# Performance work log

Hardware: AMD Instinct MI355X
Metric: run time of the kernel (lower is better)

The kernel has to match this reference:

```python
import jax, jax.numpy as jnp
import numpy as np

NUM_HEADS = 8
EPS = 1e-5

def layer_norm(x, g, b):
    m = jnp.mean(x, axis=-1, keepdims=True)
    v = jnp.mean(jnp.square(x - m), axis=-1, keepdims=True)
    return (x - m) * jax.lax.rsqrt(v + EPS) * g + b

def setup_inputs() -> dict:
    key = jax.random.key(0)
    ks = jax.random.split(key, 16)
    B, C_enc, C_dec = 2, 512, 256
    H = W = D = 16
    d_ff = 4 * C_dec
    s = 0.02
    inp = {
        'encoder_feat': jax.random.normal(ks[0], (B, C_enc, H, W, D), jnp.float32),
        'decoder_feat': jax.random.normal(ks[1], (B, C_dec, H, W, D), jnp.float32),
        # projections stored as (in, out)
        'Wq': jax.random.normal(ks[2], (C_dec, C_dec), jnp.float32) * s,
        'bq': jnp.zeros((C_dec,), jnp.float32),
        'Wk': jax.random.normal(ks[3], (C_enc, C_dec), jnp.float32) * s,
        'bk': jnp.zeros((C_dec,), jnp.float32),
        'Wv': jax.random.normal(ks[4], (C_enc, C_dec), jnp.float32) * s,
        'bv': jnp.zeros((C_dec,), jnp.float32),
        'Wo': jax.random.normal(ks[5], (C_dec, C_dec), jnp.float32) * s,
        'bo': jnp.zeros((C_dec,), jnp.float32),
        'g_enc': jnp.ones((C_enc,), jnp.float32),
        'b_enc': jnp.zeros((C_enc,), jnp.float32),
        'g_dec': jnp.ones((C_dec,), jnp.float32),
        'b_dec': jnp.zeros((C_dec,), jnp.float32),
        'g_out': jnp.ones((C_dec,), jnp.float32),
        'b_out': jnp.zeros((C_dec,), jnp.float32),
        'W1': jax.random.normal(ks[6], (C_dec, d_ff), jnp.float32) * s,
        'b1': jnp.zeros((d_ff,), jnp.float32),
        'W2': jax.random.normal(ks[7], (d_ff, C_dec), jnp.float32) * s,
        'b2': jnp.zeros((C_dec,), jnp.float32),
    }
    return inp

def reference(encoder_feat, decoder_feat, Wq, bq, Wk, bk, Wv, bv, Wo, bo,
              g_enc, b_enc, g_dec, b_dec, g_out, b_out, W1, b1, W2, b2):
    B, C_dec, H, W, D = decoder_feat.shape
    h = NUM_HEADS
    hd = C_dec // h
    scale = hd ** -0.5
    # flatten spatial dims -> sequences [B, S, C]
    enc_seq = encoder_feat.reshape(B, encoder_feat.shape[1], -1).transpose(0, 2, 1)
    dec_seq = decoder_feat.reshape(B, C_dec, -1).transpose(0, 2, 1)
    enc_n = layer_norm(enc_seq, g_enc, b_enc)
    dec_n = layer_norm(dec_seq, g_dec, b_dec)
    Sq = dec_n.shape[1]
    Sk = enc_n.shape[1]
    Q = (dec_n @ Wq + bq).reshape(B, Sq, h, hd).transpose(0, 2, 1, 3)
    K = (enc_n @ Wk + bk).reshape(B, Sk, h, hd).transpose(0, 2, 1, 3)
    V = (enc_n @ Wv + bv).reshape(B, Sk, h, hd).transpose(0, 2, 1, 3)
    attn = jnp.einsum('bhqd,bhkd->bhqk', Q, K) * scale
    attn = jax.nn.softmax(attn, axis=-1)
    out = jnp.einsum('bhqk,bhkd->bhqd', attn, V)
    out = out.transpose(0, 2, 1, 3).reshape(B, Sq, C_dec)
    out = out @ Wo + bo
    out = dec_seq + out
    ffn = jax.nn.gelu(layer_norm(out, g_out, b_out) @ W1 + b1, approximate=False) @ W2 + b2
    out = out + ffn
    return out.transpose(0, 2, 1).reshape(B, C_dec, H, W, D)
```

## Files before the change

kernel.cpp:

```cpp
#include <hip/hip_runtime.h>
#include <hip/hip_bf16.h>
#include <math.h>
#include <stdint.h>

typedef __hip_bfloat16 bf16;
typedef __attribute__((ext_vector_type(8))) short short8;
typedef __attribute__((ext_vector_type(4))) short short4v;
typedef __attribute__((ext_vector_type(4))) float f32x4;
typedef __attribute__((ext_vector_type(4))) unsigned int uint32x4;
typedef __attribute__((ext_vector_type(2))) unsigned int uint32x2;

#define B_   2
#define S_   4096
#define CE   512
#define CD   256
#define DFF  1024
#define NH   8
#define HD   32

static __device__ __forceinline__ float b2f(bf16 x) { return __bfloat162float(x); }
static __device__ __forceinline__ bf16  f2b(float x) { return __float2bfloat16(x); }
static __device__ __forceinline__ short f2bs(float x) {
  bf16 h = f2b(x); return __builtin_bit_cast(short, h);
}
static __device__ __forceinline__ float s2f(short x) {
  return b2f(__builtin_bit_cast(bf16, x));
}
static __device__ __forceinline__ bool is_f32(const unsigned* graw) {
  return graw[0] == 0x3F800000u;
}

static __device__ __forceinline__ float exp2_(float x) {
#if __has_builtin(__builtin_amdgcn_exp2f)
  return __builtin_amdgcn_exp2f(x);
#else
  float r; asm("v_exp_f32 %0, %1" : "=v"(r) : "v"(x)); return r;
#endif
}
static __device__ __forceinline__ unsigned cvt_pk_bf16(float lo, float hi) {
  unsigned r;
  asm("v_cvt_pk_bf16_f32 %0, %1, %2" : "=v"(r) : "v"(lo), "v"(hi));
  return r;
}
static __device__ __forceinline__ void perm32(unsigned& a, unsigned& b) {
#if __has_builtin(__builtin_amdgcn_permlane32_swap)
  uint32x2 r = __builtin_amdgcn_permlane32_swap(a, b, false, false);
  a = r[0]; b = r[1];
#else
  asm("v_permlane32_swap_b32 %0, %1" : "+v"(a), "+v"(b));
#endif
}
static __device__ __forceinline__ void perm16(unsigned& a, unsigned& b) {
#if __has_builtin(__builtin_amdgcn_permlane16_swap)
  uint32x2 r = __builtin_amdgcn_permlane16_swap(a, b, false, false);
  a = r[0]; b = r[1];
#else
  asm("v_permlane16_swap_b32 %0, %1" : "+v"(a), "+v"(b));
#endif
}

#define GLD16(gptr, lptr) \
  __builtin_amdgcn_global_load_lds( \
      (const __attribute__((address_space(1))) unsigned int*)(gptr), \
      (__attribute__((address_space(3))) unsigned int*)(lptr), 16, 0, 0)

#define WAITVM(N) asm volatile("s_waitcnt vmcnt(" #N ")" ::: "memory")
#define BAR() __builtin_amdgcn_s_barrier()

struct PrepTab {
  const void* tsrc[6];
  bf16* tdst[6];
  int tK[6], tsStr[6], tdStr[6];
  float tscl[6];
  int tbase[7];
  const void* csrc[14];
  bf16* cdst[14];
  float cscl[14];
  int coff[15];
};

__global__ __launch_bounds__(256) void prep_kernel(
    PrepTab p, const unsigned* __restrict__ graw) {
  __shared__ bf16 tile[32][33];
  bool f32i = is_f32(graw);
  int blk = blockIdx.x;
  if (blk < p.tbase[6]) {
    int j = 0;
    #pragma unroll 1
    while (blk >= p.tbase[j + 1]) ++j;
    int local = blk - p.tbase[j];
    int ktiles = p.tK[j] >> 5;
    int nt = local / ktiles, kt = local - nt * ktiles;
    int k0 = kt * 32, n0 = nt * 32;
    const void* src = p.tsrc[j];
    bf16* dst = p.tdst[j];
    int sStr = p.tsStr[j], dStr = p.tdStr[j];
    float scl = p.tscl[j];
    int t = threadIdx.x;
    int tc = t & 31, tr = t >> 5;
    #pragma unroll
    for (int i = 0; i < 32; i += 8) {
      size_t idx = (size_t)(k0 + tr + i) * sStr + n0 + tc;
      float v = f32i ? ((const float*)src)[idx] : b2f(((const bf16*)src)[idx]);
      tile[tr + i][tc] = f2b(v * scl);
    }
    __syncthreads();
    #pragma unroll
    for (int i = 0; i < 32; i += 8)
      dst[(size_t)(n0 + tr + i) * dStr + k0 + tc] = tile[tc][tr + i];
  } else {
    int idx = (blk - p.tbase[6]) * 256 + threadIdx.x;
    int e4 = idx * 4;
    if (e4 >= p.coff[14]) return;
    int j = 0;
    #pragma unroll 1
    while (e4 >= p.coff[j + 1]) ++j;
    int local = e4 - p.coff[j];
    float v0, v1, v2, v3;
    if (f32i) {
      float4 f = *(const float4*)((const float*)p.csrc[j] + local);
      v0 = f.x; v1 = f.y; v2 = f.z; v3 = f.w;
    } else {
      short4v h = *(const short4v*)((const short*)p.csrc[j] + local);
      v0 = s2f(h[0]); v1 = s2f(h[1]); v2 = s2f(h[2]); v3 = s2f(h[3]);
    }
    float scl = p.cscl[j];
    short4v o;
    o[0] = f2bs(v0 * scl); o[1] = f2bs(v1 * scl);
    o[2] = f2bs(v2 * scl); o[3] = f2bs(v3 * scl);
    *(short4v*)((short*)p.cdst[j] + local) = o;
  }
}

struct LNCfg {
  const bf16 *x, *g, *bt;
  bf16 *xn, *xt;
  int C;
};

template<int CC, bool XT>
static __device__ __forceinline__ void ln_tile_body(
    const LNCfg& T, int b, int s0, short* sT, short* sG, short* sBt) {
  constexpr int P = CC + 8;
  constexpr int NJ = CC / 64;
  int t = threadIdx.x;
  if (t < CC / 8)      *(short8*)&sG[t * 8] = ((const short8*)T.g)[t];
  else if (t < CC / 4) *(short8*)&sBt[(t - CC/8) * 8] = ((const short8*)T.bt)[t - CC/8];

  int cg = t >> 2;
  int sq = (t & 3) * 8;
  const short* xg = (const short*)T.x + (size_t)b * CC * S_ + s0 + sq;
  short8 ld[NJ];
  #pragma unroll
  for (int ci = 0; ci < NJ; ++ci)
    ld[ci] = *(const short8*)(xg + (size_t)(ci * 64 + cg) * S_);
  #pragma unroll
  for (int ci = 0; ci < NJ; ++ci) {
    int c = ci * 64 + cg;
    #pragma unroll
    for (int j = 0; j < 8; ++j) {
      int s = sq + j;
      sT[s * P + (c ^ ((s & 24) << 1))] = ld[ci][j];
    }
  }
  __syncthreads();

  int w = t >> 6, l = t & 63;
  int grp = l >> 3, k = l & 7;
  int s = w * 8 + grp;
  int Z = (s & 24) << 1;
  short8 vals[NJ];
  float sum = 0.f, sq2 = 0.f;
  #pragma unroll
  for (int j = 0; j < NJ; ++j) {
    vals[j] = *(const short8*)&sT[s * P + j * 64 + ((k * 8) ^ Z)];
    #pragma unroll
    for (int i = 0; i < 8; ++i) {
      float v = s2f(vals[j][i]);
      sum += v; sq2 += v * v;
    }
  }
  #pragma unroll
  for (int off = 1; off < 8; off <<= 1) {
    sum += __shfl_xor(sum, off);
    sq2 += __shfl_xor(sq2, off);
  }
  float mean = sum * (1.f / CC);
  float rstd = rsqrtf(sq2 * (1.f / CC) - mean * mean + 1e-5f);
  size_t ro = ((size_t)b * S_ + s0 + s) * CC;
  #pragma unroll
  for (int j = 0; j < NJ; ++j) {
    int c0 = j * 64 + k * 8;
    short8 gv = *(const short8*)&sG[c0];
    short8 bv = *(const short8*)&sBt[c0];
    short8 o;
    #pragma unroll
    for (int i = 0; i < 8; ++i) {
      float v = s2f(vals[j][i]);
      o[i] = f2bs((v - mean) * rstd * s2f(gv[i]) + s2f(bv[i]));
    }
    *(short8*)((short*)T.xn + ro + c0) = o;
    if (XT) *(short8*)((short*)T.xt + ro + c0) = vals[j];
  }
}

__global__ __launch_bounds__(256) void ln_tile_kernel(LNCfg e, LNCfg d) {
  __shared__ __align__(16) short sT[32 * 520];
  __shared__ __align__(16) short sG[512], sBt[512];
  int gb = blockIdx.x;
  int local = gb & 255;
  int b = local >> 7, s0 = (local & 127) * 32;
  if (gb < 256) ln_tile_body<512, false>(e, b, s0, sT, sG, sBt);
  else          ln_tile_body<256, true>(d, b, s0, sT, sG, sBt);
}

__global__ __launch_bounds__(256) void ln_rows_kernel(
    const float* __restrict__ x, const bf16* __restrict__ g,
    const bf16* __restrict__ bt, bf16* __restrict__ xn, int C) {
  int wave = threadIdx.x >> 6, lane = threadIdx.x & 63;
  int row = blockIdx.x * 4 + wave;
  float4 v = *(const float4*)(x + (size_t)row * 256 + lane * 4);
  float sum = v.x + v.y + v.z + v.w;
  float sq = v.x * v.x + v.y * v.y + v.z * v.z + v.w * v.w;
  #pragma unroll
  for (int off = 1; off < 64; off <<= 1) {
    sum += __shfl_xor(sum, off);
    sq  += __shfl_xor(sq, off);
  }
  float mean = sum * (1.f / 256.f);
  float rstd = rsqrtf(sq * (1.f / 256.f) - mean * mean + 1e-5f);
  short4v gg = *(const short4v*)((const short*)g + lane * 4);
  short4v bb = *(const short4v*)((const short*)bt + lane * 4);
  short4v o;
  o[0] = f2bs((v.x - mean) * rstd * s2f(gg[0]) + s2f(bb[0]));
  o[1] = f2bs((v.y - mean) * rstd * s2f(gg[1]) + s2f(bb[1]));
  o[2] = f2bs((v.z - mean) * rstd * s2f(gg[2]) + s2f(bb[2]));
  o[3] = f2bs((v.w - mean) * rstd * s2f(gg[3]) + s2f(bb[3]));
  *(short4v*)((short*)xn + (size_t)row * 256 + lane * 4) = o;
}

__global__ __launch_bounds__(256) void gemm_mfma_kernel(
    const bf16* __restrict__ A, const bf16* __restrict__ Wt,
    const bf16* __restrict__ bias, int M, int N, int K,
    const bf16* __restrict__ resid_bf, const float* __restrict__ resid_f,
    bf16* __restrict__ out_bf, float* __restrict__ out_f,
    void* __restrict__ out_t, const unsigned* __restrict__ graw,
    int act, int resid_mode, int out_mode) {
  __shared__ __align__(16) short sA[3][128 * 32];
  __shared__ __align__(16) short sB[3][64 * 32];
  int m0 = blockIdx.y * 128, n0 = blockIdx.x * 64;
  int t = threadIdx.x;
  int w = t >> 6;
  int wm = w >> 1, wn = w & 1;
  int n16 = t & 15, quad = (t & 63) >> 4;
  int srow = t >> 2, skg = (t & 3) * 8;

  f32x4 acc[4][2] = {};
  const short* Ag = (const short*)A;
  const short* Wg = (const short*)Wt;
  const short* a0p = Ag + (size_t)(m0 + srow) * K + skg;
  const short* a1p = Ag + (size_t)(m0 + 64 + srow) * K + skg;
  const short* wp  = Wg + (size_t)(n0 + srow) * K + skg;

  auto stage = [&](int buf, int kk) {
    GLD16(a0p + kk, (char*)sA[buf] + t * 16);
    GLD16(a1p + kk, (char*)sA[buf] + t * 16 + 4096);
    GLD16(wp + kk,  (char*)sB[buf] + t * 16);
  };
  int nt = K >> 5;
  stage(0, 0);
  stage(1, 32);
  WAITVM(3);
  BAR();

  for (int ti = 0; ti < nt; ++ti) {
    int cur = ti % 3;
    bool pf = (ti + 2) < nt;
    if (pf) stage((ti + 2) % 3, (ti + 2) * 32);
    short8 af[4], bfr[2];
    #pragma unroll
    for (int ms = 0; ms < 4; ++ms)
      af[ms] = *(const short8*)&sA[cur][(wm * 64 + ms * 16 + n16) * 32 + quad * 8];
    #pragma unroll
    for (int ns = 0; ns < 2; ++ns)
      bfr[ns] = *(const short8*)&sB[cur][(wn * 32 + ns * 16 + n16) * 32 + quad * 8];
    #pragma unroll
    for (int ms = 0; ms < 4; ++ms)
      #pragma unroll
      for (int ns = 0; ns < 2; ++ns)
        acc[ms][ns] = __builtin_amdgcn_mfma_f32_16x16x32_bf16(
            af[ms], bfr[ns], acc[ms][ns], 0, 0, 0);
    if (pf) WAITVM(3); else WAITVM(0);
    BAR();
  }

  #pragma unroll
  for (int ms = 0; ms < 4; ++ms) {
    #pragma unroll
    for (int ns = 0; ns < 2; ++ns) {
      int col = n0 + wn * 32 + ns * 16 + n16;
      float bv = b2f(bias[col]);
      #pragma unroll
      for (int r = 0; r < 4; ++r) {
        int row = m0 + wm * 64 + ms * 16 + quad * 4 + r;
        float c = acc[ms][ns][r] + bv;
        if (act == 1) c = 0.5f * c * (1.f + erff(c * 0.70710678118654752f));
        size_t off = (size_t)row * N + col;
        if (resid_mode == 1)      c += b2f(resid_bf[off]);
        else if (resid_mode == 2) c += resid_f[off];
        if (out_f) out_f[off] = c;
        else       out_bf[off] = f2b(c);
      }
    }
  }
}

__global__ __launch_bounds__(256) void gemm64_mfma_kernel(
    const bf16* __restrict__ A, const bf16* __restrict__ Wt,
    const bf16* __restrict__ bias, int M, int N, int K,
    const bf16* __restrict__ resid_bf, const float* __restrict__ resid_f,
    bf16* __restrict__ out_bf, float* __restrict__ out_f,
    void* __restrict__ out_t, const unsigned* __restrict__ graw,
    int act, int resid_mode, int out_mode) {
  __shared__ __align__(16) short sA[3][64 * 32];
  __shared__ __align__(16) short sB[3][64 * 32];
  int m0 = blockIdx.y * 64, n0 = blockIdx.x * 64;
  int t = threadIdx.x;
  int w = t >> 6;
  int wm = w >> 1, wn = w & 1;
  int n16 = t & 15, quad = (t & 63) >> 4;
  int srow = t >> 2, skg = (t & 3) * 8;

  f32x4 acc[2][2] = {};
  const short* Ag = (const short*)A;
  const short* Wg = (const short*)Wt;
  const short* ap = Ag + (size_t)(m0 + srow) * K + skg;
  const short* wp = Wg + (size_t)(n0 + srow) * K + skg;

  auto stage = [&](int buf, int kk) {
    GLD16(ap + kk, (char*)sA[buf] + t * 16);
    GLD16(wp + kk, (char*)sB[buf] + t * 16);
  };
  int nt = K >> 5;
  stage(0, 0);
  stage(1, 32);
  WAITVM(2);
  BAR();

  for (int ti = 0; ti < nt; ++ti) {
    int cur = ti % 3;
    bool pf = (ti + 2) < nt;
    if (pf) stage((ti + 2) % 3, (ti + 2) * 32);
    short8 af[2], bfr[2];
    #pragma unroll
    for (int ms = 0; ms < 2; ++ms)
      af[ms] = *(const short8*)&sA[cur][(wm * 32 + ms * 16 + n16) * 32 + quad * 8];
    #pragma unroll
    for (int ns = 0; ns < 2; ++ns)
      bfr[ns] = *(const short8*)&sB[cur][(wn * 32 + ns * 16 + n16) * 32 + quad * 8];
    #pragma unroll
    for (int ms = 0; ms < 2; ++ms)
      #pragma unroll
      for (int ns = 0; ns < 2; ++ns)
        acc[ms][ns] = __builtin_amdgcn_mfma_f32_16x16x32_bf16(
            af[ms], bfr[ns], acc[ms][ns], 0, 0, 0);
    if (pf) WAITVM(2); else WAITVM(0);
    BAR();
  }

  if (out_mode == 3) {
    bool isf32 = is_f32(graw);
    #pragma unroll
    for (int ms = 0; ms < 2; ++ms) {
      int row0 = m0 + wm * 32 + ms * 16 + quad * 4;
      int bb = row0 >> 12, s = row0 & (S_ - 1);
      #pragma unroll
      for (int ns = 0; ns < 2; ++ns) {
        int col = n0 + wn * 32 + ns * 16 + n16;
        float bv = b2f(bias[col]);
        float cv[4];
        #pragma unroll
        for (int r = 0; r < 4; ++r)
          cv[r] = acc[ms][ns][r] + bv + resid_f[(size_t)(row0 + r) * N + col];
        size_t oidx = ((size_t)bb * CD + col) * S_ + s;
        if (isf32) {
          float4 v4 = {cv[0], cv[1], cv[2], cv[3]};
          *(float4*)((float*)out_t + oidx) = v4;
        } else {
          short4v v;
          #pragma unroll
          for (int r = 0; r < 4; ++r) v[r] = f2bs(cv[r]);
          *(short4v*)((bf16*)out_t + oidx) = v;
        }
      }
    }
    return;
  }

  #pragma unroll
  for (int ms = 0; ms < 2; ++ms) {
    #pragma unroll
    for (int ns = 0; ns < 2; ++ns) {
      int col = n0 + wn * 32 + ns * 16 + n16;
      float bv = b2f(bias[col]);
      #pragma unroll
      for (int r = 0; r < 4; ++r) {
        int row = m0 + wm * 32 + ms * 16 + quad * 4 + r;
        float c = acc[ms][ns][r] + bv;
        if (act == 1) c = 0.5f * c * (1.f + erff(c * 0.70710678118654752f));
        size_t off = (size_t)row * N + col;
        if (resid_mode == 1)      c += b2f(resid_bf[off]);
        else if (resid_mode == 2) c += resid_f[off];
        if (out_f) out_f[off] = c;
        else       out_bf[off] = f2b(c);
      }
    }
  }
}

__global__ __launch_bounds__(256) void qkv_kernel(
    const bf16* __restrict__ dec_n, const bf16* __restrict__ enc_n,
    const bf16* __restrict__ Wqt, const bf16* __restrict__ Wkvt,
    const bf16* __restrict__ bq, const bf16* __restrict__ bkv,
    bf16* __restrict__ Qm, bf16* __restrict__ Km, bf16* __restrict__ VT) {
  __shared__ __align__(16) short sA[3][64 * 32];
  __shared__ __align__(16) short sB[3][64 * 32];
  bool isQ = blockIdx.x < 4;
  const short* Ag = (const short*)(isQ ? dec_n : enc_n);
  const short* Wg = (const short*)(isQ ? Wqt : Wkvt);
  const bf16* bias = isQ ? bq : bkv;
  int K = isQ ? CD : CE;
  int n0 = isQ ? blockIdx.x * 64 : (blockIdx.x - 4) * 64;
  int m0 = blockIdx.y * 64;
  int t = threadIdx.x;
  int w = t >> 6;
  int wm = w >> 1, wn = w & 1;
  int n16 = t & 15, quad = (t & 63) >> 4;
  int srow = t >> 2, skg = (t & 3) * 8;

  f32x4 acc[2][2] = {};
  const short* ap = Ag + (size_t)(m0 + srow) * K + skg;
  const short* wp = Wg + (size_t)(n0 + srow) * K + skg;
  auto stage = [&](int buf, int kk) {
    GLD16(ap + kk, (char*)sA[buf] + t * 16);
    GLD16(wp + kk, (char*)sB[buf] + t * 16);
  };
  int nt = K >> 5;
  stage(0, 0);
  stage(1, 32);
  WAITVM(2);
  BAR();

  for (int ti = 0; ti < nt; ++ti) {
    int cur = ti % 3;
    bool pf = (ti + 2) < nt;
    if (pf) stage((ti + 2) % 3, (ti + 2) * 32);
    short8 af[2], bfr[2];
    #pragma unroll
    for (int ms = 0; ms < 2; ++ms)
      af[ms] = *(const short8*)&sA[cur][(wm * 32 + ms * 16 + n16) * 32 + quad * 8];
    #pragma unroll
    for (int ns = 0; ns < 2; ++ns)
      bfr[ns] = *(const short8*)&sB[cur][(wn * 32 + ns * 16 + n16) * 32 + quad * 8];
    #pragma unroll
    for (int ms = 0; ms < 2; ++ms)
      #pragma unroll
      for (int ns = 0; ns < 2; ++ns)
        acc[ms][ns] = __builtin_amdgcn_mfma_f32_16x16x32_bf16(
            af[ms], bfr[ns], acc[ms][ns], 0, 0, 0);
    if (pf) WAITVM(2); else WAITVM(0);
    BAR();
  }

  if (!isQ && n0 >= 256) {
    #pragma unroll
    for (int ms = 0; ms < 2; ++ms) {
      int row0 = m0 + wm * 32 + ms * 16 + quad * 4;
      int bb = row0 >> 12, s = row0 & (S_ - 1);
      #pragma unroll
      for (int ns = 0; ns < 2; ++ns) {
        int col = n0 + wn * 32 + ns * 16 + n16;
        float bv = b2f(bias[col]);
        short4v v;
        #pragma unroll
        for (int r = 0; r < 4; ++r) v[r] = f2bs(acc[ms][ns][r] + bv);
        *(short4v*)(VT + ((size_t)bb * CD + col - 256) * S_ + s) = v;
      }
    }
    return;
  }
  bf16* outp = isQ ? Qm : Km;
  #pragma unroll
  for (int ms = 0; ms < 2; ++ms) {
    #pragma unroll
    for (int ns = 0; ns < 2; ++ns) {
      int col = n0 + wn * 32 + ns * 16 + n16;
      float bv = b2f(bias[col]);
      #pragma unroll
      for (int r = 0; r < 4; ++r) {
        int row = m0 + wm * 32 + ms * 16 + quad * 4 + r;
        outp[(size_t)row * CD + col] = f2b(acc[ms][ns][r] + bv);
      }
    }
  }
}

__global__ __launch_bounds__(256) void attn_mfma_kernel(
    const bf16* __restrict__ Qm, const bf16* __restrict__ Km,
    const bf16* __restrict__ VT, float* __restrict__ Op0,
    float* __restrict__ Op1, float* __restrict__ Lp) {
  __shared__ __align__(16) short sKf[2][4][64][8];
  __shared__ __align__(16) short sVt[2][32][64];
  int b = blockIdx.z, h = blockIdx.y >> 1, half = blockIdx.y & 1;
  int q0 = blockIdx.x * 128;
  int t = threadIdx.x;
  int w = t >> 6, l = t & 63;
  int n = l & 15, quad = l >> 4;
  size_t bh = ((size_t)b * S_) * CD + h * HD;
  const short* kg = (const short*)Km + bh + (size_t)(w * 16 + n) * CD + quad * 8;
  const short* vtg = (const short*)VT +
      (size_t)(b * CD + h * HD + w * 8 + (l >> 3)) * S_ + ((l & 7) ^ ((l >> 3) & 7)) * 8;

  short8 qf[2];
  #pragma unroll
  for (int f = 0; f < 2; ++f)
    qf[f] = *(const short8*)((const short*)Qm + bh +
                             (size_t)(q0 + w * 32 + f * 16 + n) * CD + quad * 8);
  short8 ones8;
  #pragma unroll
  for (int i = 0; i < 8; ++i) ones8[i] = (short)0x3F80;

  f32x4 o0[2], o1[2], ol[2];
  #pragma unroll
  for (int f = 0; f < 2; ++f) {
    o0[f] = f32x4{0.f, 0.f, 0.f, 0.f};
    o1[f] = f32x4{0.f, 0.f, 0.f, 0.f};
    ol[f] = f32x4{0.f, 0.f, 0.f, 0.f};
  }

  auto stageKV = [&](int buf, int kk) {
    GLD16(kg + (size_t)kk * CD, &sKf[buf][w][l][0]);
    GLD16(vtg + kk, (short*)sVt[buf] + w * 512 + l * 8);
  };

  int kbeg = half * (S_ / 2), kend = kbeg + S_ / 2;
  stageKV(0, kbeg);
  WAITVM(0);
  BAR();
  int cur = 0;
  for (int k0 = kbeg; k0 < kend; k0 += 64) {
    if (k0 + 64 < kend) stageKV(cur ^ 1, k0 + 64);

    f32x4 sc[2][4];
    __builtin_amdgcn_s_setprio(1);
    #pragma unroll
    for (int st = 0; st < 4; ++st) {
      short8 kf = *(const short8*)&sKf[cur][st][l][0];
      f32x4 z = {0.f, 0.f, 0.f, 0.f};
      sc[0][st] = __builtin_amdgcn_mfma_f32_16x16x32_bf16(kf, qf[0], z, 0, 0, 0);
      sc[1][st] = __builtin_amdgcn_mfma_f32_16x16x32_bf16(kf, qf[1], z, 0, 0, 0);
    }
    __builtin_amdgcn_s_setprio(0);

    short8 pf0[2], pf1[2];
    #pragma unroll
    for (int f = 0; f < 2; ++f) {
      unsigned Wd[4][2];
      #pragma unroll
      for (int st = 0; st < 4; ++st) {
        Wd[st][0] = cvt_pk_bf16(exp2_(sc[f][st][0]), exp2_(sc[f][st][1]));
        Wd[st][1] = cvt_pk_bf16(exp2_(sc[f][st][2]), exp2_(sc[f][st][3]));
      }
      uint32x4 pw0, pw1;
      #pragma unroll
      for (int m = 0; m < 2; ++m) {
        unsigned a0 = Wd[0][m], b0 = Wd[1][m];
        perm32(a0, b0); perm16(a0, b0);
        pw0[m] = a0; pw0[2 + m] = b0;
        unsigned a1 = Wd[2][m], b1 = Wd[3][m];
        perm32(a1, b1); perm16(a1, b1);
        pw1[m] = a1; pw1[2 + m] = b1;
      }
      pf0[f] = __builtin_bit_cast(short8, pw0);
      pf1[f] = __builtin_bit_cast(short8, pw1);
    }

    int p80 = quad ^ (n & 7), p81 = (4 + quad) ^ (n & 7);
    short8 v00 = *(const short8*)&sVt[cur][n][p80 * 8];
    short8 v01 = *(const short8*)&sVt[cur][n][p81 * 8];
    short8 v10 = *(const short8*)&sVt[cur][16 + n][p80 * 8];
    short8 v11 = *(const short8*)&sVt[cur][16 + n][p81 * 8];

    __builtin_amdgcn_s_setprio(1);
    #pragma unroll
    for (int f = 0; f < 2; ++f) {
      o0[f] = __builtin_amdgcn_mfma_f32_16x16x32_bf16(pf0[f], v00, o0[f], 0, 0, 0);
      o1[f] = __builtin_amdgcn_mfma_f32_16x16x32_bf16(pf0[f], v10, o1[f], 0, 0, 0);
      ol[f] = __builtin_amdgcn_mfma_f32_16x16x32_bf16(pf0[f], ones8, ol[f], 0, 0, 0);
      o0[f] = __builtin_amdgcn_mfma_f32_16x16x32_bf16(pf1[f], v01, o0[f], 0, 0, 0);
      o1[f] = __builtin_amdgcn_mfma_f32_16x16x32_bf16(pf1[f], v11, o1[f], 0, 0, 0);
      ol[f] = __builtin_amdgcn_mfma_f32_16x16x32_bf16(pf1[f], ones8, ol[f], 0, 0, 0);
    }
    __builtin_amdgcn_s_setprio(0);

    WAITVM(0);
    BAR();
    cur ^= 1;
  }

  float* Opb = half ? Op1 : Op0;
  size_t pb = (size_t)b * S_;
  #pragma unroll
  for (int f = 0; f < 2; ++f) {
    #pragma unroll
    for (int r = 0; r < 4; ++r) {
      int q = q0 + w * 32 + f * 16 + quad * 4 + r;
      float* orow = Opb + (pb + q) * CD + h * HD;
      orow[n]      = o0[f][r];
      orow[16 + n] = o1[f][r];
      if (n == 0) Lp[((size_t)(b * 2 + half) * S_ + q) * NH + h] = ol[f][r];
    }
  }
}

__global__ __launch_bounds__(256) void attn_combine_kernel(
    const float* __restrict__ Op0, const float* __restrict__ Op1,
    const float* __restrict__ Lp, bf16* __restrict__ Am) {
  int idx = blockIdx.x * 256 + threadIdx.x;
  int c = (idx * 4) & (CD - 1);
  int bs = (idx * 4) >> 8;
  int s = bs & (S_ - 1), b = bs >> 12;
  int h = c >> 5;
  size_t row = (size_t)b * S_ + s;
  float l0 = Lp[((size_t)(b * 2 + 0) * S_ + s) * NH + h];
  float l1 = Lp[((size_t)(b * 2 + 1) * S_ + s) * NH + h];
  float inv = 1.f / (l0 + l1);
  float4 a = *(const float4*)&Op0[row * CD + c];
  float4 d = *(const float4*)&Op1[row * CD + c];
  short4v v;
  v[0] = f2bs((a.x + d.x) * inv);
  v[1] = f2bs((a.y + d.y) * inv);
  v[2] = f2bs((a.z + d.z) * inv);
  v[3] = f2bs((a.w + d.w) * inv);
  *(short4v*)&Am[row * CD + c] = v;
}

extern "C" void kernel_launch(void* const* d_in, const int* in_sizes, int n_in,
                              void* d_out, int out_size, void* d_ws, size_t ws_size,
                              hipStream_t stream) {
  const float kscale = 0.25503486f;
  const unsigned* graw = (const unsigned*)d_in[10];
  char* base = (char*)d_ws;
  size_t pos = 256;

  auto alloc = [&](size_t bytes) {
    char* p = base + pos; pos = (pos + bytes + 255) & ~(size_t)255; return p;
  };
  int cidx[14] = {0, 1, 3, 5, 7, 9, 10, 11, 12, 13, 14, 15, 17, 19};
  bf16* conv[20] = {};
  for (int k = 0; k < 14; ++k) {
    int i = cidx[k];
    conv[i] = (bf16*)alloc((size_t)2 * in_sizes[i]);
  }
  bf16* Wqt  = (bf16*)alloc((size_t)CD * CD * 2);
  bf16* Wkvt = (bf16*)alloc((size_t)CE * CE * 2);
  bf16* Wot  = (bf16*)alloc((size_t)CD * CD * 2);
  bf16* W1t  = (bf16*)alloc((size_t)DFF * CD * 2);
  bf16* W2t  = (bf16*)alloc((size_t)CD * DFF * 2);
  bf16* bkv  = (bf16*)alloc((size_t)CE * 2);
  conv[5] = bkv;
  conv[7] = bkv + CD;

  bf16*  enc_n = (bf16*) alloc((size_t)B_ * S_ * CE * 2);
  bf16*  dec_n = (bf16*) alloc((size_t)B_ * S_ * CD * 2);
  bf16*  Qm    = (bf16*) alloc((size_t)B_ * S_ * CD * 2);
  bf16*  Km    = (bf16*) alloc((size_t)B_ * S_ * CD * 2);
  bf16*  VT    = (bf16*) alloc((size_t)B_ * S_ * CD * 2);
  float* outm  = (float*)alloc((size_t)B_ * S_ * CD * 4);
  bf16*  hid   = (bf16*) alloc((size_t)B_ * S_ * DFF * 2);
  float* Lp    = (float*)alloc((size_t)B_ * 2 * S_ * NH * 4);
  bf16*  Am    = dec_n;
  bf16*  ln2   = Km;
  bf16*  dec_t = (bf16*)hid;
  float* Op0   = outm;
  float* Op1   = (float*)enc_n;

  PrepTab p;
  p.tsrc[0] = d_in[2];  p.tdst[0] = Wqt;            p.tK[0] = CD;  p.tsStr[0] = CD;  p.tdStr[0] = CD;  p.tscl[0] = kscale;
  p.tsrc[1] = d_in[4];  p.tdst[1] = Wkvt;           p.tK[1] = CE;  p.tsStr[1] = CD;  p.tdStr[1] = CE;  p.tscl[1] = 1.0f;
  p.tsrc[2] = d_in[6];  p.tdst[2] = Wkvt + CD * CE; p.tK[2] = CE;  p.tsStr[2] = CD;  p.tdStr[2] = CE;  p.tscl[2] = 1.0f;
  p.tsrc[3] = d_in[8];  p.tdst[3] = Wot;            p.tK[3] = CD;  p.tsStr[3] = CD;  p.tdStr[3] = CD;  p.tscl[3] = 1.0f;
  p.tsrc[4] = d_in[16]; p.tdst[4] = W1t;            p.tK[4] = CD;  p.tsStr[4] = DFF; p.tdStr[4] = CD;  p.tscl[4] = 1.0f;
  p.tsrc[5] = d_in[18]; p.tdst[5] = W2t;            p.tK[5] = DFF; p.tsStr[5] = CD;  p.tdStr[5] = DFF; p.tscl[5] = 1.0f;
  int tN[6] = {CD, CD, CD, CD, DFF, CD};
  p.tbase[0] = 0;
  for (int j = 0; j < 6; ++j)
    p.tbase[j + 1] = p.tbase[j] + (tN[j] / 32) * (p.tK[j] / 32);
  int coff = 0;
  for (int k = 0; k < 14; ++k) {
    int i = cidx[k];
    p.csrc[k] = d_in[i];
    p.cdst[k] = conv[i];
    p.cscl[k] = (i == 3) ? kscale : 1.0f;
    p.coff[k] = coff;
    coff += in_sizes[i];
  }
  p.coff[14] = coff;
  int prep_blocks = p.tbase[6] + (coff / 4 + 255) / 256;

  const bf16* enc_c = conv[0];
  const bf16* dec_c = conv[1];
  const bf16 *bq_c = conv[3], *bo_c = conv[9];
  const bf16 *ge_c = conv[10], *be_c = conv[11];
  const bf16 *gd_c = conv[12], *bd_c = conv[13];
  const bf16 *go_c = conv[14], *bo2_c = conv[15];
  const bf16 *b1_c = conv[17], *b2_c = conv[19];

  const int M = B_ * S_;

  prep_kernel<<<prep_blocks, 256, 0, stream>>>(p, graw);

  LNCfg lne = {enc_c, ge_c, be_c, enc_n, nullptr, CE};
  LNCfg lnd = {dec_c, gd_c, bd_c, dec_n, dec_t, CD};
  ln_tile_kernel<<<512, 256, 0, stream>>>(lne, lnd);

  qkv_kernel<<<dim3(12, M / 64), 256, 0, stream>>>(
      dec_n, enc_n, Wqt, Wkvt, bq_c, bkv, Qm, Km, VT);

  attn_mfma_kernel<<<dim3(S_ / 128, NH * 2, B_), 256, 0, stream>>>(Qm, Km, VT, Op0, Op1, Lp);
  attn_combine_kernel<<<(M * CD / 4) / 256, 256, 0, stream>>>(Op0, Op1, Lp, Am);

  gemm64_mfma_kernel<<<dim3(CD / 64, M / 64), 256, 0, stream>>>(
      Am, Wot, bo_c, M, CD, CD, dec_t, nullptr, nullptr, outm, nullptr, graw, 0, 1, 0);

  ln_rows_kernel<<<dim3(M / 4), 256, 0, stream>>>(outm, go_c, bo2_c, ln2, CD);

  gemm_mfma_kernel<<<dim3(DFF / 64, M / 128), 256, 0, stream>>>(
      ln2, W1t, b1_c, M, DFF, CD, nullptr, nullptr, hid, nullptr, nullptr, graw, 1, 0, 0);
  gemm64_mfma_kernel<<<dim3(CD / 64, M / 64), 256, 0, stream>>>(
      hid, W2t, b2_c, M, CD, DFF, nullptr, outm, nullptr, nullptr, d_out, graw, 0, 0, 3);
}
```

Measured before the change: 252.2 us.

## Deepen attention K/V staging to four-buffer ring with prefetch distance two

Replaces the double-buffered K/V shared-memory staging in the attention kernel with a four-slot ring that prefetches two tiles ahead, waiting only until at most two loads are outstanding. The inner loop is unrolled by four so buffer indices are compile-time constants. This is meant to hide global-load latency better. It doubles LDS use per block, which may reduce occupancy.

```diff
diff --git a/kernel.cpp b/kernel.cpp
--- a/kernel.cpp
+++ b/kernel.cpp
@@ -509,17 +509,20 @@
     const bf16* __restrict__ Qm, const bf16* __restrict__ Km,
     const bf16* __restrict__ VT, float* __restrict__ Op0,
     float* __restrict__ Op1, float* __restrict__ Lp) {
-  __shared__ __align__(16) short sKf[2][4][64][8];
-  __shared__ __align__(16) short sVt[2][32][64];
+  __shared__ __align__(16) short sKf[4][4][64][8];
+  __shared__ __align__(16) short sVt[4][32][64];
   int b = blockIdx.z, h = blockIdx.y >> 1, half = blockIdx.y & 1;
   int q0 = blockIdx.x * 128;
   int t = threadIdx.x;
   int w = t >> 6, l = t & 63;
   int n = l & 15, quad = l >> 4;
   size_t bh = ((size_t)b * S_) * CD + h * HD;
-  const short* kg = (const short*)Km + bh + (size_t)(w * 16 + n) * CD + quad * 8;
+  int kbeg = half * (S_ / 2);
+  const int nIt = (S_ / 2) / 64;
+  const short* kg = (const short*)Km + bh + (size_t)(kbeg + w * 16 + n) * CD + quad * 8;
   const short* vtg = (const short*)VT +
-      (size_t)(b * CD + h * HD + w * 8 + (l >> 3)) * S_ + ((l & 7) ^ ((l >> 3) & 7)) * 8;
+      (size_t)(b * CD + h * HD + w * 8 + (l >> 3)) * S_ + kbeg +
+      ((l & 7) ^ ((l >> 3) & 7)) * 8;
 
   short8 qf[2];
   #pragma unroll
@@ -538,74 +541,79 @@
     ol[f] = f32x4{0.f, 0.f, 0.f, 0.f};
   }
 
-  auto stageKV = [&](int buf, int kk) {
-    GLD16(kg + (size_t)kk * CD, &sKf[buf][w][l][0]);
-    GLD16(vtg + kk, (short*)sVt[buf] + w * 512 + l * 8);
+  auto stageKV = [&](int buf, int tile) {
+    GLD16(kg + (size_t)tile * 64 * CD, &sKf[buf][w][l][0]);
+    GLD16(vtg + tile * 64, (short*)sVt[buf] + w * 512 + l * 8);
   };
 
-  int kbeg = half * (S_ / 2), kend = kbeg + S_ / 2;
-  stageKV(0, kbeg);
-  WAITVM(0);
+  stageKV(0, 0);
+  stageKV(1, 1);
+  WAITVM(2);
   BAR();
-  int cur = 0;
-  for (int k0 = kbeg; k0 < kend; k0 += 64) {
-    if (k0 + 64 < kend) stageKV(cur ^ 1, k0 + 64);
-
-    f32x4 sc[2][4];
-    __builtin_amdgcn_s_setprio(1);
-    #pragma unroll
-    for (int st = 0; st < 4; ++st) {
-      short8 kf = *(const short8*)&sKf[cur][st][l][0];
-      f32x4 z = {0.f, 0.f, 0.f, 0.f};
-      sc[0][st] = __builtin_amdgcn_mfma_f32_16x16x32_bf16(kf, qf[0], z, 0, 0, 0);
-      sc[1][st] = __builtin_amdgcn_mfma_f32_16x16x32_bf16(kf, qf[1], z, 0, 0, 0);
-    }
-    __builtin_amdgcn_s_setprio(0);
-
-    short8 pf0[2], pf1[2];
-    #pragma unroll
-    for (int f = 0; f < 2; ++f) {
-      unsigned Wd[4][2];
+
+  for (int base = 0; base < nIt; base += 4) {
+    #pragma unroll
+    for (int u = 0; u < 4; ++u) {
+      int ti = base + u;
+      const int cur = u;
+      bool pf = (ti + 2) < nIt;
+      if (pf) stageKV((u + 2) & 3, ti + 2);
+
+      f32x4 sc[2][4];
+      __builtin_amdgcn_s_setprio(1);
       #pragma unroll
       for (int st = 0; st < 4; ++st) {
-        Wd[st][0] = cvt_pk_bf16(exp2_(sc[f][st][0]), exp2_(sc[f][st][1]));
-        Wd[st][1] = cvt_pk_bf16(exp2_(sc[f][st][2]), exp2_(sc[f][st][3]));
+        short8 kf = *(const short8*)&sKf[cur][st][l][0];
+        f32x4 z = {0.f, 0.f, 0.f, 0.f};
+        sc[0][st] = __builtin_amdgcn_mfma_f32_16x16x32_bf16(kf, qf[0], z, 0, 0, 0);
+        sc[1][st] = __builtin_amdgcn_mfma_f32_16x16x32_bf16(kf, qf[1], z, 0, 0, 0);
       }
-      uint32x4 pw0, pw1;
-      #pragma unroll
-      for (int m = 0; m < 2; ++m) {
-        unsigned a0 = Wd[0][m], b0 = Wd[1][m];
-        perm32(a0, b0); perm16(a0, b0);
-        pw0[m] = a0; pw0[2 + m] = b0;
-        unsigned a1 = Wd[2][m], b1 = Wd[3][m];
-        perm32(a1, b1); perm16(a1, b1);
-        pw1[m] = a1; pw1[2 + m] = b1;
+      __builtin_amdgcn_s_setprio(0);
+
+      short8 pf0[2], pf1[2];
+      #pragma unroll
+      for (int f = 0; f < 2; ++f) {
+        unsigned Wd[4][2];
+        #pragma unroll
+        for (int st = 0; st < 4; ++st) {
+          Wd[st][0] = cvt_pk_bf16(exp2_(sc[f][st][0]), exp2_(sc[f][st][1]));
+          Wd[st][1] = cvt_pk_bf16(exp2_(sc[f][st][2]), exp2_(sc[f][st][3]));
+        }
+        uint32x4 pw0, pw1;
+        #pragma unroll
+        for (int m = 0; m < 2; ++m) {
+          unsigned a0 = Wd[0][m], b0 = Wd[1][m];
+          perm32(a0, b0); perm16(a0, b0);
+          pw0[m] = a0; pw0[2 + m] = b0;
+          unsigned a1 = Wd[2][m], b1 = Wd[3][m];
+          perm32(a1, b1); perm16(a1, b1);
+          pw1[m] = a1; pw1[2 + m] = b1;
+        }
+        pf0[f] = __builtin_bit_cast(short8, pw0);
+        pf1[f] = __builtin_bit_cast(short8, pw1);
       }
-      pf0[f] = __builtin_bit_cast(short8, pw0);
-      pf1[f] = __builtin_bit_cast(short8, pw1);
-    }
-
-    int p80 = quad ^ (n & 7), p81 = (4 + quad) ^ (n & 7);
-    short8 v00 = *(const short8*)&sVt[cur][n][p80 * 8];
-    short8 v01 = *(const short8*)&sVt[cur][n][p81 * 8];
-    short8 v10 = *(const short8*)&sVt[cur][16 + n][p80 * 8];
-    short8 v11 = *(const short8*)&sVt[cur][16 + n][p81 * 8];
-
-    __builtin_amdgcn_s_setprio(1);
-    #pragma unroll
-    for (int f = 0; f < 2; ++f) {
-      o0[f] = __builtin_amdgcn_mfma_f32_16x16x32_bf16(pf0[f], v00, o0[f], 0, 0, 0);
-      o1[f] = __builtin_amdgcn_mfma_f32_16x16x32_bf16(pf0[f], v10, o1[f], 0, 0, 0);
-      ol[f] = __builtin_amdgcn_mfma_f32_16x16x32_bf16(pf0[f], ones8, ol[f], 0, 0, 0);
-      o0[f] = __builtin_amdgcn_mfma_f32_16x16x32_bf16(pf1[f], v01, o0[f], 0, 0, 0);
-      o1[f] = __builtin_amdgcn_mfma_f32_16x16x32_bf16(pf1[f], v11, o1[f], 0, 0, 0);
-      ol[f] = __builtin_amdgcn_mfma_f32_16x16x32_bf16(pf1[f], ones8, ol[f], 0, 0, 0);
-    }
-    __builtin_amdgcn_s_setprio(0);
-
-    WAITVM(0);
-    BAR();
-    cur ^= 1;
+
+      int p80 = quad ^ (n & 7), p81 = (4 + quad) ^ (n & 7);
+      short8 v00 = *(const short8*)&sVt[cur][n][p80 * 8];
+      short8 v01 = *(const short8*)&sVt[cur][n][p81 * 8];
+      short8 v10 = *(const short8*)&sVt[cur][16 + n][p80 * 8];
+      short8 v11 = *(const short8*)&sVt[cur][16 + n][p81 * 8];
+
+      __builtin_amdgcn_s_setprio(1);
+      #pragma unroll
+      for (int f = 0; f < 2; ++f) {
+        o0[f] = __builtin_amdgcn_mfma_f32_16x16x32_bf16(pf0[f], v00, o0[f], 0, 0, 0);
+        o1[f] = __builtin_amdgcn_mfma_f32_16x16x32_bf16(pf0[f], v10, o1[f], 0, 0, 0);
+        ol[f] = __builtin_amdgcn_mfma_f32_16x16x32_bf16(pf0[f], ones8, ol[f], 0, 0, 0);
+        o0[f] = __builtin_amdgcn_mfma_f32_16x16x32_bf16(pf1[f], v01, o0[f], 0, 0, 0);
+        o1[f] = __builtin_amdgcn_mfma_f32_16x16x32_bf16(pf1[f], v11, o1[f], 0, 0, 0);
+        ol[f] = __builtin_amdgcn_mfma_f32_16x16x32_bf16(pf1[f], ones8, ol[f], 0, 0, 0);
+      }
+      __builtin_amdgcn_s_setprio(0);
+
+      if (pf) WAITVM(2); else WAITVM(0);
+      BAR();
+    }
   }
 
   float* Opb = half ? Op1 : Op0;
```

New measurement: 259.9 us. +3.1%, slower.
